# Optimization experiments

Measured on AMD Instinct MI355X. Metric: run time of the kernel, lower is better.

The kernel has to match this reference:

```python
import jax, jax.numpy as jnp
import numpy as np

B, T, C = 4, 2048, 1024
N_HEAD = 16
HEAD_DIM = C // N_HEAD


def setup_inputs() -> dict:
    key = jax.random.key(0)
    ks = jax.random.split(key, 5)
    bound = 1.0 / np.sqrt(C)
    x = jax.random.normal(ks[0], (B, T, C), dtype=jnp.float32)
    W_attn = jax.random.uniform(ks[1], (C, 3 * C), minval=-bound, maxval=bound, dtype=jnp.float32)
    b_attn = jax.random.uniform(ks[2], (3 * C,), minval=-bound, maxval=bound, dtype=jnp.float32)
    W_proj = jax.random.uniform(ks[3], (C, C), minval=-bound, maxval=bound, dtype=jnp.float32)
    b_proj = jax.random.uniform(ks[4], (C,), minval=-bound, maxval=bound, dtype=jnp.float32)
    return {"x": x, "W_attn": W_attn, "b_attn": b_attn, "W_proj": W_proj, "b_proj": b_proj}


def reference(x, W_attn, b_attn, W_proj, b_proj):
    Bx, Tx, Cx = x.shape
    qkv = x @ W_attn + b_attn                       # [B,T,3C]
    q, k, v = jnp.split(qkv, 3, axis=2)
    # [B,T,C] -> [B,H,T,D]
    q = q.reshape(Bx, Tx, N_HEAD, HEAD_DIM).transpose(0, 2, 1, 3)
    k = k.reshape(Bx, Tx, N_HEAD, HEAD_DIM).transpose(0, 2, 1, 3)
    v = v.reshape(Bx, Tx, N_HEAD, HEAD_DIM).transpose(0, 2, 1, 3)
    scale = 1.0 / np.sqrt(HEAD_DIM).astype(np.float32)
    att = jnp.einsum('bhqd,bhkd->bhqk', q, k) * scale   # [B,H,T,T]
    causal = jnp.tril(jnp.ones((Tx, Tx), dtype=bool))
    att = jnp.where(causal[None, None], att, -jnp.inf)
    att = jax.nn.softmax(att, axis=-1)
    y = jnp.einsum('bhqk,bhkd->bhqd', att, v)           # [B,H,T,D]
    y = y.transpose(0, 2, 1, 3).reshape(Bx, Tx, Cx)
    return y @ W_proj + b_proj
```

## Files before the change

kernel.cpp:

```cpp
#include <hip/hip_runtime.h>

#define Bsz 4
#define Tn 2048
#define Cn 1024
#define Hn 16
#define Dn 64
#define Mn (Bsz * Tn)
#define NQKV (3 * Cn)
#define BH (Bsz * Hn)

typedef short bf16x8_t __attribute__((ext_vector_type(8)));
typedef float f32x4 __attribute__((ext_vector_type(4)));

static __device__ __forceinline__ float exp2_fast(float x) {
    return __builtin_amdgcn_exp2f(x);
}

static __device__ __forceinline__ unsigned short f2bf(float f) {
    union { float f; unsigned int u; } v; v.f = f;
    unsigned int r = v.u + 0x7FFFu + ((v.u >> 16) & 1u);
    return (unsigned short)(r >> 16);
}

static __device__ __forceinline__ unsigned int fbits(float f) {
    union { float f; unsigned int u; } v; v.f = f; return v.u;
}

static __device__ __forceinline__ bf16x8_t ld_frag(const unsigned short* p) {
    bf16x8_t r;
    *reinterpret_cast<float4*>(&r) = *reinterpret_cast<const float4*>(p);
    return r;
}

#define ASYNC_COPY16(gp, lp)                                                         \
    __builtin_amdgcn_global_load_lds((__attribute__((address_space(1))) void*)(gp),  \
                                     (__attribute__((address_space(3))) void*)(lp),  \
                                     16, 0, 0)

__global__ void cast_f32_bf16(const float* __restrict__ src,
                              unsigned short* __restrict__ dst, int n4) {
    int i = blockIdx.x * blockDim.x + threadIdx.x;
    if (i < n4) {
        float4 v = reinterpret_cast<const float4*>(src)[i];
        ushort4 o;
        o.x = f2bf(v.x); o.y = f2bf(v.y); o.z = f2bf(v.z); o.w = f2bf(v.w);
        reinterpret_cast<ushort4*>(dst)[i] = o;
    }
}

__global__ void transpose_cast(const float* __restrict__ src,
                               unsigned short* __restrict__ dst, int R, int Cc) {
    __shared__ float tile[32][33];
    int c0 = blockIdx.x * 32, r0 = blockIdx.y * 32;
    int tx = threadIdx.x & 31, ty = threadIdx.x >> 5;
#pragma unroll
    for (int i = 0; i < 4; i++)
        tile[ty + i * 8][tx] = src[(long)(r0 + ty + i * 8) * Cc + c0 + tx];
    __syncthreads();
#pragma unroll
    for (int i = 0; i < 4; i++)
        dst[(long)(c0 + ty + i * 8) * R + r0 + tx] = f2bf(tile[tx][ty + i * 8]);
}

template <int MODE>
__global__ __launch_bounds__(256) void gemm128(const unsigned short* __restrict__ A,
                                               const unsigned short* __restrict__ Bt,
                                               const float* __restrict__ bias,
                                               float* __restrict__ outF,
                                               unsigned short* __restrict__ Qb,
                                               unsigned short* __restrict__ Kb,
                                               unsigned short* __restrict__ Vt,
                                               int M, int N, int Kd) {
    __shared__ __align__(16) unsigned short As[128 * 32];
    __shared__ __align__(16) unsigned short Bs[128 * 32];
    int n0 = blockIdx.x * 128, m0 = blockIdx.y * 128;
    int tid = threadIdx.x;
    int lane = tid & 63, w = tid >> 6;
    int wm = w >> 1, wn = w & 1;
    int quad = lane >> 4, l15 = lane & 15;
    int r = lane >> 2, c = lane & 3;

    const unsigned short* AgBase = A + (long)(m0 + w * 32 + r) * Kd + c * 8;
    const unsigned short* BgBase = Bt + (long)(n0 + w * 32 + r) * Kd + c * 8;
    unsigned short* ldsA = As + (w * 32) * 32;
    unsigned short* ldsB = Bs + (w * 32) * 32;

    f32x4 acc[4][4] = {};

    for (int kb = 0; kb < Kd; kb += 32) {
        ASYNC_COPY16(AgBase + kb, ldsA);
        ASYNC_COPY16(AgBase + 16 * Kd + kb, ldsA + 512);
        ASYNC_COPY16(BgBase + kb, ldsB);
        ASYNC_COPY16(BgBase + 16 * Kd + kb, ldsB + 512);
        __syncthreads();
        bf16x8_t af[4], bfr[4];
#pragma unroll
        for (int i = 0; i < 4; i++)
            af[i] = ld_frag(&As[(wm * 64 + i * 16 + l15) * 32 + quad * 8]);
#pragma unroll
        for (int j = 0; j < 4; j++)
            bfr[j] = ld_frag(&Bs[(wn * 64 + j * 16 + l15) * 32 + quad * 8]);
#pragma unroll
        for (int i = 0; i < 4; i++)
#pragma unroll
            for (int j = 0; j < 4; j++)
                acc[i][j] = __builtin_amdgcn_mfma_f32_16x16x32_bf16(af[i], bfr[j], acc[i][j], 0, 0, 0);
        __syncthreads();
    }

#pragma unroll
    for (int i = 0; i < 4; i++)
#pragma unroll
        for (int j = 0; j < 4; j++) {
            int col = n0 + wn * 64 + j * 16 + l15;
            float bval = bias[col];
#pragma unroll
            for (int rr = 0; rr < 4; rr++) {
                int row = m0 + wm * 64 + i * 16 + quad * 4 + rr;
                float val = acc[i][j][rr] + bval;
                if (MODE == 0) {
                    outF[(long)row * N + col] = val;
                } else {
                    int seg = col >> 10, within = col & 1023;
                    int h = within >> 6, d = within & 63;
                    int b = row >> 11, t = row & 2047;
                    int bh = b * Hn + h;
                    if (seg == 0) {
                        Qb[((long)bh * Tn + t) * Dn + d] = f2bf(val * 0.18033688f);
                    } else if (seg == 1) {
                        Kb[((long)bh * Tn + t) * Dn + d] = f2bf(val);
                    } else {
                        Vt[((long)bh * Dn + d) * Tn + t] = f2bf(val);
                    }
                }
            }
        }
}

__global__ __launch_bounds__(256) void attn_kernel(const unsigned short* __restrict__ Qb,
                                                   const unsigned short* __restrict__ Kb,
                                                   const unsigned short* __restrict__ Vt,
                                                   unsigned short* __restrict__ Yb) {
    __shared__ __align__(16) unsigned short Ks[64 * 72];
    __shared__ __align__(16) unsigned short Vs[64 * 72];
    __shared__ __align__(16) unsigned short Plds[4][2][16 * 72];
    int tid = threadIdx.x, w = tid >> 6, lane = tid & 63;
    int quad = lane >> 4, l15 = lane & 15;

    int flat = blockIdx.y * 16 + blockIdx.x;
    int xcd = flat & 7, slot = flat >> 3;
    int bh = xcd * 8 + (slot >> 4);
    int qi = 15 - (slot & 15);
    int b = bh >> 4, h = bh & 15;

    int q0b = qi * 128;
    int nt = 2 * qi + 2;

    const unsigned short* Qh = Qb + (long)bh * Tn * Dn;
    const unsigned short* Kh = Kb + (long)bh * Tn * Dn;
    const unsigned short* Vh = Vt + (long)bh * Dn * Tn;

    int sr = tid >> 3;
    int sc = (tid & 7) * 8;

    bf16x8_t qf[2][2];
#pragma unroll
    for (int h2 = 0; h2 < 2; h2++) {
        int qrow = q0b + h2 * 64 + w * 16 + l15;
        qf[h2][0] = ld_frag(&Qh[qrow * Dn + quad * 8]);
        qf[h2][1] = ld_frag(&Qh[qrow * Dn + 32 + quad * 8]);
    }

    float l_acc[2] = {0.f, 0.f};
    f32x4 Of[2][4] = {};

    float4 kr0 = *reinterpret_cast<const float4*>(&Kh[sr * Dn + sc]);
    float4 kr1 = *reinterpret_cast<const float4*>(&Kh[(32 + sr) * Dn + sc]);
    float4 vr0 = *reinterpret_cast<const float4*>(&Vh[sr * Tn + sc]);
    float4 vr1 = *reinterpret_cast<const float4*>(&Vh[(32 + sr) * Tn + sc]);

#pragma unroll 1
    for (int t = 0; t < nt; t++) {
        int kt0 = t * 64;
        __syncthreads();
        *reinterpret_cast<float4*>(&Ks[sr * 72 + sc]) = kr0;
        *reinterpret_cast<float4*>(&Ks[(32 + sr) * 72 + sc]) = kr1;
        *reinterpret_cast<float4*>(&Vs[sr * 72 + sc]) = vr0;
        *reinterpret_cast<float4*>(&Vs[(32 + sr) * 72 + sc]) = vr1;
        if (t + 1 < nt) {
            int kn = kt0 + 64;
            kr0 = *reinterpret_cast<const float4*>(&Kh[(kn + sr) * Dn + sc]);
            kr1 = *reinterpret_cast<const float4*>(&Kh[(kn + 32 + sr) * Dn + sc]);
            vr0 = *reinterpret_cast<const float4*>(&Vh[sr * Tn + kn + sc]);
            vr1 = *reinterpret_cast<const float4*>(&Vh[(32 + sr) * Tn + kn + sc]);
        }
        __syncthreads();

        bool act0 = (kt0 <= q0b);

        f32x4 st[2][4];
        __builtin_amdgcn_s_setprio(1);
#pragma unroll
        for (int ti = 0; ti < 4; ti++) {
            bf16x8_t ka0 = ld_frag(&Ks[(ti * 16 + l15) * 72 + quad * 8]);
            bf16x8_t ka1 = ld_frag(&Ks[(ti * 16 + l15) * 72 + 32 + quad * 8]);
            if (act0) {
                f32x4 z = {};
                z = __builtin_amdgcn_mfma_f32_16x16x32_bf16(ka0, qf[0][0], z, 0, 0, 0);
                st[0][ti] = __builtin_amdgcn_mfma_f32_16x16x32_bf16(ka1, qf[0][1], z, 0, 0, 0);
            }
            f32x4 z1 = {};
            z1 = __builtin_amdgcn_mfma_f32_16x16x32_bf16(ka0, qf[1][0], z1, 0, 0, 0);
            st[1][ti] = __builtin_amdgcn_mfma_f32_16x16x32_bf16(ka1, qf[1][1], z1, 0, 0, 0);
        }
        __builtin_amdgcn_s_setprio(0);

        bf16x8_t pa[2][2];
#pragma unroll
        for (int h2 = 0; h2 < 2; h2++) {
            int qbase = q0b + h2 * 64;
            if (h2 == 0 && !act0) continue;
            if (kt0 == qbase) {
                int q_glob = qbase + w * 16 + l15;
#pragma unroll
                for (int ti = 0; ti < 4; ti++)
#pragma unroll
                    for (int rr = 0; rr < 4; rr++)
                        if (kt0 + ti * 16 + quad * 4 + rr > q_glob) st[h2][ti][rr] = -1e30f;
            }
            float lsum = 0.f;
#pragma unroll
            for (int ti = 0; ti < 4; ti++)
#pragma unroll
                for (int rr = 0; rr < 4; rr++) {
                    float e = exp2_fast(st[h2][ti][rr]);
                    st[h2][ti][rr] = e;
                    lsum += e;
                }
            l_acc[h2] += lsum;
            unsigned short* Pw = &Plds[w][h2][0];
#pragma unroll
            for (int ti = 0; ti < 4; ti++) {
                unsigned u0 = fbits(st[h2][ti][0]) + 0x8000u;
                unsigned u1 = fbits(st[h2][ti][1]) + 0x8000u;
                unsigned u2 = fbits(st[h2][ti][2]) + 0x8000u;
                unsigned u3 = fbits(st[h2][ti][3]) + 0x8000u;
                uint2 pk;
                pk.x = __builtin_amdgcn_perm(u1, u0, 0x07060302);
                pk.y = __builtin_amdgcn_perm(u3, u2, 0x07060302);
                *reinterpret_cast<uint2*>(&Pw[l15 * 72 + ti * 16 + quad * 4]) = pk;
            }
#pragma unroll
            for (int kc = 0; kc < 2; kc++)
                pa[h2][kc] = ld_frag(&Pw[l15 * 72 + kc * 32 + quad * 8]);
        }

        __builtin_amdgcn_s_setprio(1);
#pragma unroll
        for (int kc = 0; kc < 2; kc++)
#pragma unroll
            for (int dt = 0; dt < 4; dt++) {
                bf16x8_t vb = ld_frag(&Vs[(dt * 16 + l15) * 72 + kc * 32 + quad * 8]);
                if (act0)
                    Of[0][dt] = __builtin_amdgcn_mfma_f32_16x16x32_bf16(pa[0][kc], vb, Of[0][dt], 0, 0, 0);
                Of[1][dt] = __builtin_amdgcn_mfma_f32_16x16x32_bf16(pa[1][kc], vb, Of[1][dt], 0, 0, 0);
            }
        __builtin_amdgcn_s_setprio(0);
    }

#pragma unroll
    for (int h2 = 0; h2 < 2; h2++) {
        float l_tot = l_acc[h2];
        l_tot += __shfl_xor(l_tot, 16);
        l_tot += __shfl_xor(l_tot, 32);
        int qw = q0b + h2 * 64 + w * 16;
#pragma unroll
        for (int rr = 0; rr < 4; rr++) {
            float linv = 1.f / __shfl(l_tot, quad * 4 + rr);
            int t = qw + quad * 4 + rr;
            long rowbase = ((long)(b * Tn + t)) * Cn + h * Dn;
#pragma unroll
            for (int dt = 0; dt < 4; dt++)
                Yb[rowbase + dt * 16 + l15] = f2bf(Of[h2][dt][rr] * linv);
        }
    }
}

extern "C" void kernel_launch(void* const* d_in, const int* in_sizes, int n_in,
                              void* d_out, int out_size, void* d_ws, size_t ws_size,
                              hipStream_t stream) {
    const float* x      = (const float*)d_in[0];
    const float* W_attn = (const float*)d_in[1];
    const float* b_attn = (const float*)d_in[2];
    const float* W_proj = (const float*)d_in[3];
    const float* b_proj = (const float*)d_in[4];
    float* out = (float*)d_out;

    unsigned short* xb      = (unsigned short*)d_ws;
    unsigned short* Wqkv_t  = xb + (size_t)Mn * Cn;
    unsigned short* Wproj_t = Wqkv_t + (size_t)NQKV * Cn;
    unsigned short* Qb      = Wproj_t + (size_t)Cn * Cn;
    unsigned short* Kb      = Qb + (size_t)BH * Tn * Dn;
    unsigned short* Vt      = Kb + (size_t)BH * Tn * Dn;
    unsigned short* Yb      = Vt + (size_t)BH * Tn * Dn;

    cast_f32_bf16<<<(Mn * Cn / 4 + 255) / 256, 256, 0, stream>>>(x, xb, Mn * Cn / 4);
    transpose_cast<<<dim3(NQKV / 32, Cn / 32), 256, 0, stream>>>(W_attn, Wqkv_t, Cn, NQKV);
    transpose_cast<<<dim3(Cn / 32, Cn / 32), 256, 0, stream>>>(W_proj, Wproj_t, Cn, Cn);

    gemm128<1><<<dim3(NQKV / 128, Mn / 128), 256, 0, stream>>>(
        xb, Wqkv_t, b_attn, nullptr, Qb, Kb, Vt, Mn, NQKV, Cn);

    attn_kernel<<<dim3(16, BH), 256, 0, stream>>>(Qb, Kb, Vt, Yb);

    gemm128<0><<<dim3(Cn / 128, Mn / 128), 256, 0, stream>>>(
        Yb, Wproj_t, b_proj, out, nullptr, nullptr, nullptr, Mn, Cn, Cn);
}
```

Before: 311.5 us.

## Process paired 64-row query tiles sequentially per block for causal load balance

Each block now handles two 64-row query tiles (pr and 31-pr) one after another instead of one 128-row tile, giving every block the same total number of key tiles. This evens out work across blocks under the causal mask. The trade-off is that each K/V tile loaded into shared memory feeds one 64-row query block instead of two, so LDS and global traffic per unit of compute roughly doubles and there is less MFMA work between barriers.

```diff
diff --git a/kernel.cpp b/kernel.cpp
--- a/kernel.cpp
+++ b/kernel.cpp
@@ -143,18 +143,15 @@
                                                    unsigned short* __restrict__ Yb) {
     __shared__ __align__(16) unsigned short Ks[64 * 72];
     __shared__ __align__(16) unsigned short Vs[64 * 72];
-    __shared__ __align__(16) unsigned short Plds[4][2][16 * 72];
+    __shared__ __align__(16) unsigned short Plds[4][16 * 72];
     int tid = threadIdx.x, w = tid >> 6, lane = tid & 63;
     int quad = lane >> 4, l15 = lane & 15;
 
     int flat = blockIdx.y * 16 + blockIdx.x;
     int xcd = flat & 7, slot = flat >> 3;
     int bh = xcd * 8 + (slot >> 4);
-    int qi = 15 - (slot & 15);
+    int pr = slot & 15;
     int b = bh >> 4, h = bh & 15;
-
-    int q0b = qi * 128;
-    int nt = 2 * qi + 2;
 
     const unsigned short* Qh = Qb + (long)bh * Tn * Dn;
     const unsigned short* Kh = Kb + (long)bh * Tn * Dn;
@@ -163,117 +160,103 @@
     int sr = tid >> 3;
     int sc = (tid & 7) * 8;
 
-    bf16x8_t qf[2][2];
-#pragma unroll
-    for (int h2 = 0; h2 < 2; h2++) {
-        int qrow = q0b + h2 * 64 + w * 16 + l15;
-        qf[h2][0] = ld_frag(&Qh[qrow * Dn + quad * 8]);
-        qf[h2][1] = ld_frag(&Qh[qrow * Dn + 32 + quad * 8]);
-    }
-
-    float l_acc[2] = {0.f, 0.f};
-    f32x4 Of[2][4] = {};
-
-    float4 kr0 = *reinterpret_cast<const float4*>(&Kh[sr * Dn + sc]);
-    float4 kr1 = *reinterpret_cast<const float4*>(&Kh[(32 + sr) * Dn + sc]);
-    float4 vr0 = *reinterpret_cast<const float4*>(&Vh[sr * Tn + sc]);
-    float4 vr1 = *reinterpret_cast<const float4*>(&Vh[(32 + sr) * Tn + sc]);
-
 #pragma unroll 1
-    for (int t = 0; t < nt; t++) {
-        int kt0 = t * 64;
-        __syncthreads();
-        *reinterpret_cast<float4*>(&Ks[sr * 72 + sc]) = kr0;
-        *reinterpret_cast<float4*>(&Ks[(32 + sr) * 72 + sc]) = kr1;
-        *reinterpret_cast<float4*>(&Vs[sr * 72 + sc]) = vr0;
-        *reinterpret_cast<float4*>(&Vs[(32 + sr) * 72 + sc]) = vr1;
-        if (t + 1 < nt) {
-            int kn = kt0 + 64;
-            kr0 = *reinterpret_cast<const float4*>(&Kh[(kn + sr) * Dn + sc]);
-            kr1 = *reinterpret_cast<const float4*>(&Kh[(kn + 32 + sr) * Dn + sc]);
-            vr0 = *reinterpret_cast<const float4*>(&Vh[sr * Tn + kn + sc]);
-            vr1 = *reinterpret_cast<const float4*>(&Vh[(32 + sr) * Tn + kn + sc]);
-        }
-        __syncthreads();
-
-        bool act0 = (kt0 <= q0b);
-
-        f32x4 st[2][4];
-        __builtin_amdgcn_s_setprio(1);
-#pragma unroll
-        for (int ti = 0; ti < 4; ti++) {
-            bf16x8_t ka0 = ld_frag(&Ks[(ti * 16 + l15) * 72 + quad * 8]);
-            bf16x8_t ka1 = ld_frag(&Ks[(ti * 16 + l15) * 72 + 32 + quad * 8]);
-            if (act0) {
+    for (int s = 0; s < 2; s++) {
+        int qi2 = s ? pr : (31 - pr);
+        int qbase = qi2 * 64;
+        int nt = qi2 + 1;
+
+        int qrow = qbase + w * 16 + l15;
+        bf16x8_t qf0 = ld_frag(&Qh[qrow * Dn + quad * 8]);
+        bf16x8_t qf1 = ld_frag(&Qh[qrow * Dn + 32 + quad * 8]);
+
+        float l_acc = 0.f;
+        f32x4 Of[4] = {};
+
+        float4 kr0 = *reinterpret_cast<const float4*>(&Kh[sr * Dn + sc]);
+        float4 kr1 = *reinterpret_cast<const float4*>(&Kh[(32 + sr) * Dn + sc]);
+        float4 vr0 = *reinterpret_cast<const float4*>(&Vh[sr * Tn + sc]);
+        float4 vr1 = *reinterpret_cast<const float4*>(&Vh[(32 + sr) * Tn + sc]);
+
+#pragma unroll 1
+        for (int t = 0; t < nt; t++) {
+            int kt0 = t * 64;
+            __syncthreads();
+            *reinterpret_cast<float4*>(&Ks[sr * 72 + sc]) = kr0;
+            *reinterpret_cast<float4*>(&Ks[(32 + sr) * 72 + sc]) = kr1;
+            *reinterpret_cast<float4*>(&Vs[sr * 72 + sc]) = vr0;
+            *reinterpret_cast<float4*>(&Vs[(32 + sr) * 72 + sc]) = vr1;
+            if (t + 1 < nt) {
+                int kn = kt0 + 64;
+                kr0 = *reinterpret_cast<const float4*>(&Kh[(kn + sr) * Dn + sc]);
+                kr1 = *reinterpret_cast<const float4*>(&Kh[(kn + 32 + sr) * Dn + sc]);
+                vr0 = *reinterpret_cast<const float4*>(&Vh[sr * Tn + kn + sc]);
+                vr1 = *reinterpret_cast<const float4*>(&Vh[(32 + sr) * Tn + kn + sc]);
+            }
+            __syncthreads();
+
+            f32x4 st[4];
+            __builtin_amdgcn_s_setprio(1);
+#pragma unroll
+            for (int ti = 0; ti < 4; ti++) {
+                bf16x8_t ka0 = ld_frag(&Ks[(ti * 16 + l15) * 72 + quad * 8]);
+                bf16x8_t ka1 = ld_frag(&Ks[(ti * 16 + l15) * 72 + 32 + quad * 8]);
                 f32x4 z = {};
-                z = __builtin_amdgcn_mfma_f32_16x16x32_bf16(ka0, qf[0][0], z, 0, 0, 0);
-                st[0][ti] = __builtin_amdgcn_mfma_f32_16x16x32_bf16(ka1, qf[0][1], z, 0, 0, 0);
-            }
-            f32x4 z1 = {};
-            z1 = __builtin_amdgcn_mfma_f32_16x16x32_bf16(ka0, qf[1][0], z1, 0, 0, 0);
-            st[1][ti] = __builtin_amdgcn_mfma_f32_16x16x32_bf16(ka1, qf[1][1], z1, 0, 0, 0);
-        }
-        __builtin_amdgcn_s_setprio(0);
-
-        bf16x8_t pa[2][2];
-#pragma unroll
-        for (int h2 = 0; h2 < 2; h2++) {
-            int qbase = q0b + h2 * 64;
-            if (h2 == 0 && !act0) continue;
-            if (kt0 == qbase) {
+                z = __builtin_amdgcn_mfma_f32_16x16x32_bf16(ka0, qf0, z, 0, 0, 0);
+                st[ti] = __builtin_amdgcn_mfma_f32_16x16x32_bf16(ka1, qf1, z, 0, 0, 0);
+            }
+            __builtin_amdgcn_s_setprio(0);
+
+            if (t == nt - 1) {
                 int q_glob = qbase + w * 16 + l15;
 #pragma unroll
                 for (int ti = 0; ti < 4; ti++)
 #pragma unroll
                     for (int rr = 0; rr < 4; rr++)
-                        if (kt0 + ti * 16 + quad * 4 + rr > q_glob) st[h2][ti][rr] = -1e30f;
-            }
+                        if (kt0 + ti * 16 + quad * 4 + rr > q_glob) st[ti][rr] = -1e30f;
+            }
+
             float lsum = 0.f;
 #pragma unroll
             for (int ti = 0; ti < 4; ti++)
 #pragma unroll
                 for (int rr = 0; rr < 4; rr++) {
-                    float e = exp2_fast(st[h2][ti][rr]);
-                    st[h2][ti][rr] = e;
+                    float e = exp2_fast(st[ti][rr]);
+                    st[ti][rr] = e;
                     lsum += e;
                 }
-            l_acc[h2] += lsum;
-            unsigned short* Pw = &Plds[w][h2][0];
+            l_acc += lsum;
+
+            unsigned short* Pw = &Plds[w][0];
 #pragma unroll
             for (int ti = 0; ti < 4; ti++) {
-                unsigned u0 = fbits(st[h2][ti][0]) + 0x8000u;
-                unsigned u1 = fbits(st[h2][ti][1]) + 0x8000u;
-                unsigned u2 = fbits(st[h2][ti][2]) + 0x8000u;
-                unsigned u3 = fbits(st[h2][ti][3]) + 0x8000u;
+                unsigned u0 = fbits(st[ti][0]) + 0x8000u;
+                unsigned u1 = fbits(st[ti][1]) + 0x8000u;
+                unsigned u2 = fbits(st[ti][2]) + 0x8000u;
+                unsigned u3 = fbits(st[ti][3]) + 0x8000u;
                 uint2 pk;
                 pk.x = __builtin_amdgcn_perm(u1, u0, 0x07060302);
                 pk.y = __builtin_amdgcn_perm(u3, u2, 0x07060302);
                 *reinterpret_cast<uint2*>(&Pw[l15 * 72 + ti * 16 + quad * 4]) = pk;
             }
-#pragma unroll
-            for (int kc = 0; kc < 2; kc++)
-                pa[h2][kc] = ld_frag(&Pw[l15 * 72 + kc * 32 + quad * 8]);
+            bf16x8_t pa0 = ld_frag(&Pw[l15 * 72 + quad * 8]);
+            bf16x8_t pa1 = ld_frag(&Pw[l15 * 72 + 32 + quad * 8]);
+
+            __builtin_amdgcn_s_setprio(1);
+#pragma unroll
+            for (int dt = 0; dt < 4; dt++) {
+                bf16x8_t vb0 = ld_frag(&Vs[(dt * 16 + l15) * 72 + quad * 8]);
+                bf16x8_t vb1 = ld_frag(&Vs[(dt * 16 + l15) * 72 + 32 + quad * 8]);
+                Of[dt] = __builtin_amdgcn_mfma_f32_16x16x32_bf16(pa0, vb0, Of[dt], 0, 0, 0);
+                Of[dt] = __builtin_amdgcn_mfma_f32_16x16x32_bf16(pa1, vb1, Of[dt], 0, 0, 0);
+            }
+            __builtin_amdgcn_s_setprio(0);
         }
 
-        __builtin_amdgcn_s_setprio(1);
-#pragma unroll
-        for (int kc = 0; kc < 2; kc++)
-#pragma unroll
-            for (int dt = 0; dt < 4; dt++) {
-                bf16x8_t vb = ld_frag(&Vs[(dt * 16 + l15) * 72 + kc * 32 + quad * 8]);
-                if (act0)
-                    Of[0][dt] = __builtin_amdgcn_mfma_f32_16x16x32_bf16(pa[0][kc], vb, Of[0][dt], 0, 0, 0);
-                Of[1][dt] = __builtin_amdgcn_mfma_f32_16x16x32_bf16(pa[1][kc], vb, Of[1][dt], 0, 0, 0);
-            }
-        __builtin_amdgcn_s_setprio(0);
-    }
-
-#pragma unroll
-    for (int h2 = 0; h2 < 2; h2++) {
-        float l_tot = l_acc[h2];
+        float l_tot = l_acc;
         l_tot += __shfl_xor(l_tot, 16);
         l_tot += __shfl_xor(l_tot, 32);
-        int qw = q0b + h2 * 64 + w * 16;
+        int qw = qbase + w * 16;
 #pragma unroll
         for (int rr = 0; rr < 4; rr++) {
             float linv = 1.f / __shfl(l_tot, quad * 4 + rr);
@@ -281,7 +264,7 @@
             long rowbase = ((long)(b * Tn + t)) * Cn + h * Dn;
 #pragma unroll
             for (int dt = 0; dt < 4; dt++)
-                Yb[rowbase + dt * 16 + l15] = f2bf(Of[h2][dt][rr] * linv);
+                Yb[rowbase + dt * 16 + l15] = f2bf(Of[dt][rr] * linv);
         }
     }
 }
```

Measured after the change: 295.1 us. 5.3% less time.
